# Kernel optimization log

Measured on AMD Instinct MI355X. Metric: run time of the kernel, lower is better.

## Reference

```python
import math
import jax, jax.numpy as jnp
import numpy as np

B, T, H, D = 8, 4096, 8, 64
D_MODEL = H * D  # 512
K = 8            # multiwavelet order k
C = 64           # channel multiplier c (c*k = d_model)
CK = C * K
MODES = 32       # num_modes (alpha)
L = 2            # decomposition levels


def _skft(z, w_re, w_im):
    # sparseKernelFT1d: (B, N, c, k) -> (B, N, c, k)
    b, n, c, k = z.shape
    zf = jnp.fft.rfft(z.reshape(b, n, c * k).transpose(0, 2, 1), axis=-1)  # (b, ck, n//2+1)
    f = n // 2 + 1
    l = min(MODES, f)
    w = w_re[:, :, :l] + 1j * w_im[:, :, :l]
    out = jnp.einsum('bix,iox->box', zf[:, :, :l], w)
    out_ft = jnp.pad(out, ((0, 0), (0, 0), (0, f - l)))  # zero out high modes
    y = jnp.fft.irfft(out_ft, n=n, axis=-1)
    return y.transpose(0, 2, 1).reshape(b, n, c, k)


def _pad_pow2(z):
    n = z.shape[1]
    nl = 2 ** math.ceil(math.log2(n))
    if n == nl:
        return z
    return jnp.concatenate([z, z[:, : nl - n]], axis=1)


def _forward(x, lin_in_w, lin_in_b, lin_out_w, lin_out_b, t0_w, t0_b,
             wA_re, wA_im, wB_re, wB_im, wC_re, wC_im, ec_s, ec_d, rc_e, rc_o):
    b, t, h, d = x.shape
    z = x.reshape(b, t, h * d) @ lin_in_w + lin_in_b  # (b, t, c*k)
    z = z.reshape(b, t, C, K)
    n0 = z.shape[1]
    z = _pad_pow2(z)
    Ud, Us = [], []
    cur = z
    for _ in range(L):  # decompose
        xa = jnp.concatenate([cur[:, ::2], cur[:, 1::2]], axis=-1)  # (b, n/2, c, 2k)
        dcoef = xa @ ec_d  # (b, n/2, c, k)
        scoef = xa @ ec_s
        Ud.append(_skft(dcoef, wA_re, wA_im) + _skft(scoef, wB_re, wB_im))
        Us.append(_skft(dcoef, wC_re, wC_im))
        cur = scoef
    cur = cur @ t0_w + t0_b  # T_0: Linear(k, k) on last dim
    for i in range(L - 1, -1, -1):  # reconstruct, coarsest -> finest
        cur = cur + Us[i]
        cur = jnp.concatenate([cur, Ud[i]], axis=-1)  # (b, n, c, 2k)
        x_e = cur @ rc_e
        x_o = cur @ rc_o
        bb, nn, cc, kk = x_e.shape
        cur = jnp.stack([x_e, x_o], axis=2).reshape(bb, 2 * nn, cc, kk)  # interleave even/odd
    cur = cur[:, :n0]
    out = cur.reshape(b, t, CK) @ lin_out_w + lin_out_b
    return out.reshape(b, t, h, d)


def setup_inputs():
    key = jax.random.key(0)
    ks = jax.random.split(key, 18)
    scale = 1.0 / (CK * CK)  # matches 1/(c*k*c*k)
    u = lambda kk: scale * jax.random.uniform(kk, (CK, CK, MODES), jnp.float32)
    return {
        'x': jax.random.normal(ks[0], (B, T, H, D), jnp.float32),
        'lin_in_w': jax.random.normal(ks[1], (D_MODEL, CK), jnp.float32) * 0.02,
        'lin_in_b': jnp.zeros((CK,), jnp.float32),
        'lin_out_w': jax.random.normal(ks[2], (CK, D_MODEL), jnp.float32) * 0.02,
        'lin_out_b': jnp.zeros((D_MODEL,), jnp.float32),
        't0_w': jax.random.normal(ks[3], (K, K), jnp.float32) * 0.3,
        't0_b': jnp.zeros((K,), jnp.float32),
        'wA_re': u(ks[4]), 'wA_im': u(ks[5]),
        'wB_re': u(ks[6]), 'wB_im': u(ks[7]),
        'wC_re': u(ks[8]), 'wC_im': u(ks[9]),
        'ec_s': jax.random.normal(ks[10], (2 * K, K), jnp.float32) * 0.35,
        'ec_d': jax.random.normal(ks[11], (2 * K, K), jnp.float32) * 0.35,
        'rc_e': jax.random.normal(ks[12], (2 * K, K), jnp.float32) * 0.35,
        'rc_o': jax.random.normal(ks[13], (2 * K, K), jnp.float32) * 0.35,
    }


def reference(x, lin_in_w, lin_in_b, lin_out_w, lin_out_b, t0_w, t0_b,
              wA_re, wA_im, wB_re, wB_im, wC_re, wC_im, ec_s, ec_d, rc_e, rc_o):
    return _forward(x, lin_in_w, lin_in_b, lin_out_w, lin_out_b, t0_w, t0_b,
                    wA_re, wA_im, wB_re, wB_im, wC_re, wC_im, ec_s, ec_d, rc_e, rc_o)
```

## Files before the change

kernel.cpp:

```cpp
#include <hip/hip_runtime.h>
#include <math.h>

constexpr int NB = 8;
constexpr int CKN = 512;
constexpr int NMODE = 32;

typedef __attribute__((ext_vector_type(8))) short short8x;
typedef __attribute__((ext_vector_type(4))) float f32x4;

__device__ inline unsigned short f2bf(float f) {
  union { float f; unsigned u; } v; v.f = f;
  unsigned u = v.u;
  unsigned r = (u + 0x7fffu + ((u >> 16) & 1u)) >> 16;
  return (unsigned short)r;
}

__global__ void build_tables(float* __restrict__ tab, int n) {
  int idx = blockIdx.x * 256 + threadIdx.x;
  if (idx >= n * NMODE) return;
  int t = idx >> 5;
  int x = idx & 31;
  long long tx = ((long long)t * (long long)x) % n;
  double th = 6.28318530717958647692529 * (double)tx / (double)n;
  tab[2 * idx]     = (float)cos(th);
  tab[2 * idx + 1] = (float)sin(th);
}

__global__ __launch_bounds__(256) void gemm_mfma(
    const float* __restrict__ A, const float* __restrict__ W,
    const float* __restrict__ bias, float* __restrict__ C) {
  __shared__ __align__(16) unsigned short As[128 * 40];
  __shared__ __align__(16) unsigned short Bs[128 * 40];
  const int bm = blockIdx.x * 128, bn = blockIdx.y * 128;
  const int tid = threadIdx.x;
  const int wave = tid >> 6, lane = tid & 63;
  const int wm = (wave >> 1) * 64, wn = (wave & 1) * 64;
  const int lm = lane & 15, quad = lane >> 4;

  f32x4 zero = {0.f, 0.f, 0.f, 0.f};
  f32x4 acc[4][4];
#pragma unroll
  for (int i = 0; i < 4; ++i)
#pragma unroll
    for (int j = 0; j < 4; ++j) acc[i][j] = zero;

  for (int k0 = 0; k0 < 512; k0 += 32) {
    __syncthreads();
#pragma unroll
    for (int r = 0; r < 4; ++r) {
      int slot = tid + r * 256;
      int m = slot >> 3, k4 = (slot & 7) << 2;
      float4 v = *(const float4*)&A[(size_t)(bm + m) * 512 + k0 + k4];
      ushort4 u;
      u.x = f2bf(v.x); u.y = f2bf(v.y); u.z = f2bf(v.z); u.w = f2bf(v.w);
      *(ushort4*)&As[m * 40 + k4] = u;
    }
#pragma unroll
    for (int r = 0; r < 4; ++r) {
      int slot = tid + r * 256;
      int n = slot & 127, kg = slot >> 7;
      float w0 = W[(size_t)(k0 + kg * 4 + 0) * 512 + bn + n];
      float w1 = W[(size_t)(k0 + kg * 4 + 1) * 512 + bn + n];
      float w2 = W[(size_t)(k0 + kg * 4 + 2) * 512 + bn + n];
      float w3 = W[(size_t)(k0 + kg * 4 + 3) * 512 + bn + n];
      ushort4 u;
      u.x = f2bf(w0); u.y = f2bf(w1); u.z = f2bf(w2); u.w = f2bf(w3);
      *(ushort4*)&Bs[n * 40 + kg * 4] = u;
    }
    __syncthreads();
    short8x af[4], bf[4];
#pragma unroll
    for (int ti = 0; ti < 4; ++ti)
      af[ti] = *(short8x*)&As[(wm + ti * 16 + lm) * 40 + quad * 8];
#pragma unroll
    for (int tj = 0; tj < 4; ++tj)
      bf[tj] = *(short8x*)&Bs[(wn + tj * 16 + lm) * 40 + quad * 8];
#pragma unroll
    for (int ti = 0; ti < 4; ++ti)
#pragma unroll
      for (int tj = 0; tj < 4; ++tj)
        acc[ti][tj] = __builtin_amdgcn_mfma_f32_16x16x32_bf16(af[ti], bf[tj], acc[ti][tj], 0, 0, 0);
  }
  float bv[4];
#pragma unroll
  for (int tj = 0; tj < 4; ++tj) bv[tj] = bias[bn + wn + tj * 16 + lm];
#pragma unroll
  for (int ti = 0; ti < 4; ++ti)
#pragma unroll
    for (int tj = 0; tj < 4; ++tj)
#pragma unroll
      for (int r = 0; r < 4; ++r)
        C[(size_t)(bm + wm + ti * 16 + quad * 4 + r) * 512 + bn + wn + tj * 16 + lm] =
            acc[ti][tj][r] + bv[tj];
}

__global__ __launch_bounds__(256) void coef_kernel(
    const float* __restrict__ cur, const float* __restrict__ ecd,
    const float* __restrict__ ecs, float* __restrict__ dcoef,
    float* __restrict__ scoef, int nhalf) {
  __shared__ float wd[128], ws2[128];
  int tid = threadIdx.x;
  if (tid < 128) { wd[tid] = ecd[tid]; ws2[tid] = ecs[tid]; }
  __syncthreads();
  size_t idx = (size_t)blockIdx.x * 256 + tid;
  int c = (int)(idx & 63);
  int t = (int)((idx >> 6) % (size_t)nhalf);
  int b = (int)(idx / ((size_t)nhalf * 64));
  const float* r0 = cur + ((size_t)b * nhalf * 2 + 2 * (size_t)t) * CKN + c * 8;
  float xa[16];
  *(float4*)&xa[0]  = *(const float4*)&r0[0];
  *(float4*)&xa[4]  = *(const float4*)&r0[4];
  *(float4*)&xa[8]  = *(const float4*)&r0[CKN];
  *(float4*)&xa[12] = *(const float4*)&r0[CKN + 4];
  float d[8] = {}, s[8] = {};
#pragma unroll
  for (int j = 0; j < 16; ++j) {
    float v = xa[j];
#pragma unroll
    for (int k = 0; k < 8; ++k) {
      d[k] += v * wd[j * 8 + k];
      s[k] += v * ws2[j * 8 + k];
    }
  }
  size_t o = ((size_t)b * nhalf + t) * CKN + c * 8;
  *(float4*)&dcoef[o]     = *(float4*)&d[0];
  *(float4*)&dcoef[o + 4] = *(float4*)&d[4];
  *(float4*)&scoef[o]     = *(float4*)&s[0];
  *(float4*)&scoef[o + 4] = *(float4*)&s[4];
}

__global__ __launch_bounds__(256) void fwd_dft_partial(
    const float* __restrict__ in, const float* __restrict__ tab,
    float* __restrict__ part, int n) {
  __shared__ float ltab[64 * 64];
  const int p = blockIdx.x, b = blockIdx.y;
  const int P = gridDim.x;
  const int tid = threadIdx.x;
  for (int i = tid; i < 4096; i += 256) ltab[i] = tab[(size_t)p * 4096 + i];
  __syncthreads();
  float ar0[NMODE] = {}, ai0[NMODE] = {}, ar1[NMODE] = {}, ai1[NMODE] = {};
  const float* src = in + ((size_t)b * n + (size_t)p * 64) * CKN + 2 * tid;
#pragma unroll 2
  for (int t = 0; t < 64; ++t) {
    float2 v = *(const float2*)&src[(size_t)t * CKN];
    const float* tr = &ltab[t * 64];
#pragma unroll
    for (int x = 0; x < NMODE; ++x) {
      float c = tr[2 * x], sn = tr[2 * x + 1];
      ar0[x] += v.x * c; ai0[x] -= v.x * sn;
      ar1[x] += v.y * c; ai1[x] -= v.y * sn;
    }
  }
  float* pr = part + ((size_t)b * P + p) * NMODE * CKN + 2 * tid;
  float* pi = pr + (size_t)NB * P * NMODE * CKN;
#pragma unroll
  for (int x = 0; x < NMODE; ++x) {
    float2 r; r.x = ar0[x]; r.y = ar1[x];
    float2 im; im.x = ai0[x]; im.y = ai1[x];
    *(float2*)&pr[(size_t)x * CKN] = r;
    *(float2*)&pi[(size_t)x * CKN] = im;
  }
}

__global__ __launch_bounds__(256) void dft_reduce(
    const float* __restrict__ part, float* __restrict__ fre,
    float* __restrict__ fim, int P) {
  int idx = blockIdx.x * 256 + threadIdx.x;
  int ck = idx & 511;
  int x = (idx >> 9) & 31;
  int b = idx >> 14;
  size_t base = ((size_t)b * P * NMODE + x) * CKN + ck;
  size_t ip = (size_t)NB * P * NMODE * CKN;
  size_t ps = (size_t)NMODE * CKN;
  float sr = 0.f, si = 0.f;
  for (int p = 0; p < P; ++p) { sr += part[base + p * ps]; si += part[base + ip + p * ps]; }
  fre[idx] = sr;
  fim[idx] = si;
}

__global__ __launch_bounds__(256) void mode_mul(
    const float* __restrict__ freq,
    const float* __restrict__ wAre, const float* __restrict__ wAim,
    const float* __restrict__ wBre, const float* __restrict__ wBim,
    const float* __restrict__ wCre, const float* __restrict__ wCim,
    float* __restrict__ mpart) {
  __shared__ __align__(16) float lf[4096];
  const int otile = blockIdx.x, chunk = blockIdx.y;
  const int tid = threadIdx.x;
  const int x = tid & 31, ol = tid >> 5;
  const int o = otile * 8 + ol;
  const int i0 = chunk * 32;
  float acc[2][8][4] = {};
  for (int ii = 0; ii < 32; ii += 4) {
    float wv[4][6];
    size_t wo0 = ((size_t)(i0 + ii) * 512 + o) * 32 + x;
#pragma unroll
    for (int i = 0; i < 4; ++i) {
      size_t wo = wo0 + (size_t)i * 16384;
      wv[i][0] = wAre[wo]; wv[i][1] = wAim[wo];
      wv[i][2] = wBre[wo]; wv[i][3] = wBim[wo];
      wv[i][4] = wCre[wo]; wv[i][5] = wCim[wo];
    }
    __syncthreads();
#pragma unroll
    for (int j = 0; j < 16; ++j) {
      int idx = tid + j * 256;
      int il = idx & 3, xx = (idx >> 2) & 31, bb = (idx >> 7) & 7;
      int pl = (idx >> 10) & 3, lv = idx >> 12;
      lf[(((lv * 8 + bb) * 4 + il) * 32 + xx) * 4 + pl] =
          freq[(size_t)(lv * 4 + pl) * 131072 + ((size_t)bb * 32 + xx) * 512 + i0 + ii + il];
    }
    __syncthreads();
#pragma unroll
    for (int i = 0; i < 4; ++i) {
      float aR = wv[i][0], aI = wv[i][1];
      float bR = wv[i][2], bI = wv[i][3];
      float cR = wv[i][4], cI = wv[i][5];
#pragma unroll
      for (int lv = 0; lv < 2; ++lv)
#pragma unroll
        for (int bq = 0; bq < 8; ++bq) {
          float4 f = *(float4*)&lf[(((lv * 8 + bq) * 4 + i) * 32 + x) * 4];
          acc[lv][bq][0] += f.x * aR - f.y * aI + f.z * bR - f.w * bI;
          acc[lv][bq][1] += f.x * aI + f.y * aR + f.z * bI + f.w * bR;
          acc[lv][bq][2] += f.x * cR - f.y * cI;
          acc[lv][bq][3] += f.x * cI + f.y * cR;
        }
    }
  }
#pragma unroll
  for (int lv = 0; lv < 2; ++lv)
#pragma unroll
    for (int bq = 0; bq < 8; ++bq) {
      float4 v;
      v.x = acc[lv][bq][0]; v.y = acc[lv][bq][1];
      v.z = acc[lv][bq][2]; v.w = acc[lv][bq][3];
      *(float4*)&mpart[((((size_t)lv * 16 + chunk) * 8 + bq) * 32 + x) * 2048 + o * 4] = v;
    }
}

__global__ __launch_bounds__(256) void mm_reduce(
    const float* __restrict__ mpart, float* __restrict__ outplanes) {
  int idx = blockIdx.x * 256 + threadIdx.x;
  int o = idx & 511;
  int x = (idx >> 9) & 31;
  int b = (idx >> 14) & 7;
  int lvl = idx >> 17;
  float s0 = 0, s1 = 0, s2 = 0, s3 = 0;
  for (int ch = 0; ch < 16; ++ch) {
    const float4 v = *(const float4*)&mpart[((((size_t)lvl * 16 + ch) * 8 + b) * 32 + x) * 2048 + o * 4];
    s0 += v.x; s1 += v.y; s2 += v.z; s3 += v.w;
  }
  size_t fo = ((size_t)b * 32 + x) * 512 + o;
  float* bp = outplanes + (size_t)lvl * 4 * 131072;
  bp[fo] = s0;
  bp[131072 + fo] = s1;
  bp[262144 + fo] = s2;
  bp[393216 + fo] = s3;
}

__global__ __launch_bounds__(256) void t0_kernel(
    float* __restrict__ cur, const float* __restrict__ w,
    const float* __restrict__ bvec, int rows) {
  __shared__ float lw[64];
  __shared__ float lb[8];
  int tid = threadIdx.x;
  if (tid < 64) lw[tid] = w[tid];
  if (tid < 8) lb[tid] = bvec[tid];
  __syncthreads();
  size_t r = (size_t)blockIdx.x * 256 + tid;
  if (r >= (size_t)rows) return;
  float* p = cur + r * 8;
  float in[8];
  *(float4*)&in[0] = *(const float4*)&p[0];
  *(float4*)&in[4] = *(const float4*)&p[4];
  float outv[8];
#pragma unroll
  for (int k2 = 0; k2 < 8; ++k2) {
    float a = lb[k2];
#pragma unroll
    for (int k = 0; k < 8; ++k) a += in[k] * lw[k * 8 + k2];
    outv[k2] = a;
  }
  *(float4*)&p[0] = *(float4*)&outv[0];
  *(float4*)&p[4] = *(float4*)&outv[4];
}

__global__ __launch_bounds__(256) void inv_dft(
    const float* __restrict__ fre, const float* __restrict__ fim,
    const float* __restrict__ tab, float* __restrict__ out,
    int n, int beta) {
  __shared__ float ltab[512];
  const int tg = blockIdx.x, b = blockIdx.y;
  const int tid = threadIdx.x;
  for (int i = tid; i < 512; i += 256) ltab[i] = tab[(size_t)tg * 512 + i];
  __syncthreads();
  const int o = tid * 2;
  const float invn = 1.0f / (float)n;
  float fr0[NMODE], fi0[NMODE], fr1[NMODE], fi1[NMODE];
  const float* pr = fre + (size_t)b * NMODE * CKN + o;
  const float* pi = fim + (size_t)b * NMODE * CKN + o;
#pragma unroll
  for (int x = 0; x < NMODE; ++x) {
    float w = (x == 0) ? invn : 2.0f * invn;
    float2 r = *(const float2*)&pr[(size_t)x * CKN];
    float2 im = *(const float2*)&pi[(size_t)x * CKN];
    fr0[x] = r.x * w; fr1[x] = r.y * w;
    fi0[x] = im.x * w; fi1[x] = im.y * w;
  }
  float* dst = out + ((size_t)b * n + (size_t)tg * 8) * CKN + o;
#pragma unroll
  for (int t = 0; t < 8; ++t) {
    const float* tr = &ltab[t * 64];
    float y0 = 0.f, y1 = 0.f;
#pragma unroll
    for (int x = 0; x < NMODE; ++x) {
      float c = tr[2 * x], sn = tr[2 * x + 1];
      y0 += fr0[x] * c - fi0[x] * sn;
      y1 += fr1[x] * c - fi1[x] * sn;
    }
    float2* dp = (float2*)&dst[(size_t)t * CKN];
    float2 yy;
    if (beta) { float2 prev = *dp; yy.x = prev.x + y0; yy.y = prev.y + y1; }
    else { yy.x = y0; yy.y = y1; }
    *dp = yy;
  }
}

__global__ __launch_bounds__(256) void recon_kernel(
    const float* __restrict__ cur, const float* __restrict__ ud,
    const float* __restrict__ rce, const float* __restrict__ rco,
    float* __restrict__ out, int n) {
  __shared__ float we[128], wo[128];
  int tid = threadIdx.x;
  if (tid < 128) { we[tid] = rce[tid]; wo[tid] = rco[tid]; }
  __syncthreads();
  size_t idx = (size_t)blockIdx.x * 256 + tid;
  int c = (int)(idx & 63);
  int t = (int)((idx >> 6) % (size_t)n);
  int b = (int)(idx / ((size_t)n * 64));
  size_t off = ((size_t)b * n + t) * CKN + c * 8;
  float cat[16];
  *(float4*)&cat[0]  = *(const float4*)&cur[off];
  *(float4*)&cat[4]  = *(const float4*)&cur[off + 4];
  *(float4*)&cat[8]  = *(const float4*)&ud[off];
  *(float4*)&cat[12] = *(const float4*)&ud[off + 4];
  float xe[8] = {}, xo[8] = {};
#pragma unroll
  for (int j = 0; j < 16; ++j) {
    float v = cat[j];
#pragma unroll
    for (int k = 0; k < 8; ++k) {
      xe[k] += v * we[j * 8 + k];
      xo[k] += v * wo[j * 8 + k];
    }
  }
  size_t po = ((size_t)b * 2 * n + 2 * (size_t)t) * CKN + c * 8;
  *(float4*)&out[po]           = *(float4*)&xe[0];
  *(float4*)&out[po + 4]       = *(float4*)&xe[4];
  *(float4*)&out[po + CKN]     = *(float4*)&xo[0];
  *(float4*)&out[po + CKN + 4] = *(float4*)&xo[4];
}

extern "C" void kernel_launch(void* const* d_in, const int* in_sizes, int n_in,
                              void* d_out, int out_size, void* d_ws, size_t ws_size,
                              hipStream_t stream) {
  (void)in_sizes; (void)n_in; (void)out_size; (void)ws_size;
  const float* x         = (const float*)d_in[0];
  const float* lin_in_w  = (const float*)d_in[1];
  const float* lin_in_b  = (const float*)d_in[2];
  const float* lin_out_w = (const float*)d_in[3];
  const float* lin_out_b = (const float*)d_in[4];
  const float* t0_w      = (const float*)d_in[5];
  const float* t0_b      = (const float*)d_in[6];
  const float* wAre      = (const float*)d_in[7];
  const float* wAim      = (const float*)d_in[8];
  const float* wBre      = (const float*)d_in[9];
  const float* wBim      = (const float*)d_in[10];
  const float* wCre      = (const float*)d_in[11];
  const float* wCim      = (const float*)d_in[12];
  const float* ec_s      = (const float*)d_in[13];
  const float* ec_d      = (const float*)d_in[14];
  const float* rc_e      = (const float*)d_in[15];
  const float* rc_o      = (const float*)d_in[16];
  float* ws = (float*)d_ws;
  float* out = (float*)d_out;

  float* Z    = ws + 0;
  float* D0   = ws + 16777216;
  float* S0   = ws + 25165824;
  float* D1   = ws + 33554432;
  float* S1   = ws + 37748736;
  float* F0   = ws + 41943040;
  float* TAB2 = ws + 44040192;
  float* TAB1 = ws + 44171264;
  float* PART = Z;
  float* MMP  = Z;

  build_tables<<<(2048 * NMODE + 255) / 256, 256, 0, stream>>>(TAB2, 2048);
  build_tables<<<(1024 * NMODE + 255) / 256, 256, 0, stream>>>(TAB1, 1024);

  gemm_mfma<<<dim3(256, 4), 256, 0, stream>>>(x, lin_in_w, lin_in_b, Z);

  coef_kernel<<<(NB * 2048 * 64) / 256, 256, 0, stream>>>(Z, ec_d, ec_s, D0, S0, 2048);

  fwd_dft_partial<<<dim3(32, NB), 256, 0, stream>>>(D0, TAB2, PART, 2048);
  dft_reduce<<<512, 256, 0, stream>>>(PART, F0 + 0 * 131072, F0 + 1 * 131072, 32);
  fwd_dft_partial<<<dim3(32, NB), 256, 0, stream>>>(S0, TAB2, PART, 2048);
  dft_reduce<<<512, 256, 0, stream>>>(PART, F0 + 2 * 131072, F0 + 3 * 131072, 32);

  coef_kernel<<<(NB * 1024 * 64) / 256, 256, 0, stream>>>(S0, ec_d, ec_s, D1, S1, 1024);

  fwd_dft_partial<<<dim3(16, NB), 256, 0, stream>>>(D1, TAB1, PART, 1024);
  dft_reduce<<<512, 256, 0, stream>>>(PART, F0 + 4 * 131072, F0 + 5 * 131072, 16);
  fwd_dft_partial<<<dim3(16, NB), 256, 0, stream>>>(S1, TAB1, PART, 1024);
  dft_reduce<<<512, 256, 0, stream>>>(PART, F0 + 6 * 131072, F0 + 7 * 131072, 16);

  mode_mul<<<dim3(64, 16), 256, 0, stream>>>(F0, wAre, wAim, wBre, wBim, wCre, wCim, MMP);
  mm_reduce<<<1024, 256, 0, stream>>>(MMP, F0 + 8 * 131072);

  t0_kernel<<<(NB * 1024 * 64) / 256, 256, 0, stream>>>(S1, t0_w, t0_b, NB * 1024 * 64);

  inv_dft<<<dim3(128, NB), 256, 0, stream>>>(F0 + 14 * 131072, F0 + 15 * 131072, TAB1, S1, 1024, 1);
  inv_dft<<<dim3(128, NB), 256, 0, stream>>>(F0 + 12 * 131072, F0 + 13 * 131072, TAB1, D1, 1024, 0);
  recon_kernel<<<(NB * 1024 * 64) / 256, 256, 0, stream>>>(S1, D1, rc_e, rc_o, S0, 1024);

  inv_dft<<<dim3(256, NB), 256, 0, stream>>>(F0 + 10 * 131072, F0 + 11 * 131072, TAB2, S0, 2048, 1);
  inv_dft<<<dim3(256, NB), 256, 0, stream>>>(F0 + 8 * 131072, F0 + 9 * 131072, TAB2, D0, 2048, 0);
  recon_kernel<<<(NB * 2048 * 64) / 256, 256, 0, stream>>>(S0, D0, rc_e, rc_o, Z, 2048);

  gemm_mfma<<<dim3(256, 4), 256, 0, stream>>>(Z, lin_out_w, lin_out_b, out);
}
```

Measured before the change: 899.1 us.

## Replace twiddle tables with on-the-fly rotation recurrences and retile DFT and mode-mul kernels

```diff
diff --git a/kernel.cpp b/kernel.cpp
--- a/kernel.cpp
+++ b/kernel.cpp
@@ -4,6 +4,7 @@
 constexpr int NB = 8;
 constexpr int CKN = 512;
 constexpr int NMODE = 32;
+constexpr int NCH = 8;
 
 typedef __attribute__((ext_vector_type(8))) short short8x;
 typedef __attribute__((ext_vector_type(4))) float f32x4;
@@ -13,17 +14,6 @@
   unsigned u = v.u;
   unsigned r = (u + 0x7fffu + ((u >> 16) & 1u)) >> 16;
   return (unsigned short)r;
-}
-
-__global__ void build_tables(float* __restrict__ tab, int n) {
-  int idx = blockIdx.x * 256 + threadIdx.x;
-  if (idx >= n * NMODE) return;
-  int t = idx >> 5;
-  int x = idx & 31;
-  long long tx = ((long long)t * (long long)x) % n;
-  double th = 6.28318530717958647692529 * (double)tx / (double)n;
-  tab[2 * idx]     = (float)cos(th);
-  tab[2 * idx + 1] = (float)sin(th);
 }
 
 __global__ __launch_bounds__(256) void gemm_mfma(
@@ -129,37 +119,42 @@
   *(float4*)&scoef[o + 4] = *(float4*)&s[4];
 }
 
-__global__ __launch_bounds__(256) void fwd_dft_partial(
-    const float* __restrict__ in, const float* __restrict__ tab,
-    float* __restrict__ part, int n) {
-  __shared__ float ltab[64 * 64];
-  const int p = blockIdx.x, b = blockIdx.y;
+__global__ __launch_bounds__(256) void fwd_dft(
+    const float* __restrict__ in, float* __restrict__ part, int n) {
+  const int p = blockIdx.x, b = blockIdx.y, cb = blockIdx.z;
   const int P = gridDim.x;
   const int tid = threadIdx.x;
-  for (int i = tid; i < 4096; i += 256) ltab[i] = tab[(size_t)p * 4096 + i];
-  __syncthreads();
-  float ar0[NMODE] = {}, ai0[NMODE] = {}, ar1[NMODE] = {}, ai1[NMODE] = {};
-  const float* src = in + ((size_t)b * n + (size_t)p * 64) * CKN + 2 * tid;
-#pragma unroll 2
+  const int cs = tid & 7, x = tid >> 3;
+  const int ck = cb * 64 + cs * 8;
+  const int t0 = p * 64;
+  float c, s, cstep, sstep;
+  float a0 = -6.28318530717958647692f * (float)((x * t0) % n) / (float)n;
+  __sincosf(a0, &s, &c);
+  float a1 = -6.28318530717958647692f * (float)x / (float)n;
+  __sincosf(a1, &sstep, &cstep);
+  float ar[8] = {}, ai[8] = {};
+  const float* src = in + ((size_t)b * n + t0) * CKN + ck;
   for (int t = 0; t < 64; ++t) {
-    float2 v = *(const float2*)&src[(size_t)t * CKN];
-    const float* tr = &ltab[t * 64];
-#pragma unroll
-    for (int x = 0; x < NMODE; ++x) {
-      float c = tr[2 * x], sn = tr[2 * x + 1];
-      ar0[x] += v.x * c; ai0[x] -= v.x * sn;
-      ar1[x] += v.y * c; ai1[x] -= v.y * sn;
-    }
-  }
-  float* pr = part + ((size_t)b * P + p) * NMODE * CKN + 2 * tid;
+    float4 v0 = *(const float4*)&src[(size_t)t * CKN];
+    float4 v1 = *(const float4*)&src[(size_t)t * CKN + 4];
+    ar[0] += v0.x * c; ai[0] += v0.x * s;
+    ar[1] += v0.y * c; ai[1] += v0.y * s;
+    ar[2] += v0.z * c; ai[2] += v0.z * s;
+    ar[3] += v0.w * c; ai[3] += v0.w * s;
+    ar[4] += v1.x * c; ai[4] += v1.x * s;
+    ar[5] += v1.y * c; ai[5] += v1.y * s;
+    ar[6] += v1.z * c; ai[6] += v1.z * s;
+    ar[7] += v1.w * c; ai[7] += v1.w * s;
+    float cn = c * cstep - s * sstep;
+    float sn = c * sstep + s * cstep;
+    c = cn; s = sn;
+  }
+  float* pr = part + (((size_t)b * P + p) * NMODE + x) * CKN + ck;
   float* pi = pr + (size_t)NB * P * NMODE * CKN;
-#pragma unroll
-  for (int x = 0; x < NMODE; ++x) {
-    float2 r; r.x = ar0[x]; r.y = ar1[x];
-    float2 im; im.x = ai0[x]; im.y = ai1[x];
-    *(float2*)&pr[(size_t)x * CKN] = r;
-    *(float2*)&pi[(size_t)x * CKN] = im;
-  }
+  *(float4*)&pr[0] = *(float4*)&ar[0];
+  *(float4*)&pr[4] = *(float4*)&ar[4];
+  *(float4*)&pi[0] = *(float4*)&ai[0];
+  *(float4*)&pi[4] = *(float4*)&ai[4];
 }
 
 __global__ __launch_bounds__(256) void dft_reduce(
@@ -184,71 +179,84 @@
     const float* __restrict__ wBre, const float* __restrict__ wBim,
     const float* __restrict__ wCre, const float* __restrict__ wCim,
     float* __restrict__ mpart) {
-  __shared__ __align__(16) float lf[4096];
+  __shared__ __align__(16) float lf[8192];
   const int otile = blockIdx.x, chunk = blockIdx.y;
   const int tid = threadIdx.x;
-  const int x = tid & 31, ol = tid >> 5;
-  const int o = otile * 8 + ol;
-  const int i0 = chunk * 32;
-  float acc[2][8][4] = {};
-  for (int ii = 0; ii < 32; ii += 4) {
-    float wv[4][6];
-    size_t wo0 = ((size_t)(i0 + ii) * 512 + o) * 32 + x;
-#pragma unroll
-    for (int i = 0; i < 4; ++i) {
-      size_t wo = wo0 + (size_t)i * 16384;
-      wv[i][0] = wAre[wo]; wv[i][1] = wAim[wo];
-      wv[i][2] = wBre[wo]; wv[i][3] = wBim[wo];
-      wv[i][4] = wCre[wo]; wv[i][5] = wCim[wo];
-    }
+  const int wave = tid >> 6, lane = tid & 63;
+  const int x = lane & 31, og = lane >> 5;
+  const int r0 = wave * 4;
+  const int i0 = chunk * 64;
+  const int o0 = otile * 4 + og * 2;
+  const int sx = tid & 31, spl = (tid >> 5) & 3, srp = tid >> 7;
+  float acc[4][2][4] = {};
+  for (int ii = 0; ii < 64; ii += 4) {
     __syncthreads();
 #pragma unroll
-    for (int j = 0; j < 16; ++j) {
-      int idx = tid + j * 256;
-      int il = idx & 3, xx = (idx >> 2) & 31, bb = (idx >> 7) & 7;
-      int pl = (idx >> 10) & 3, lv = idx >> 12;
-      lf[(((lv * 8 + bb) * 4 + il) * 32 + xx) * 4 + pl] =
-          freq[(size_t)(lv * 4 + pl) * 131072 + ((size_t)bb * 32 + xx) * 512 + i0 + ii + il];
+    for (int j = 0; j < 8; ++j) {
+      int row = srp * 8 + j;
+      int lv = row >> 3, bb = row & 7;
+      float4 v = *(const float4*)&freq[(size_t)(lv * 4 + spl) * 131072 +
+                                       ((size_t)bb * 32 + sx) * 512 + i0 + ii];
+      *(float4*)&lf[((row * 4 + spl) * 32 + sx) * 4] = v;
     }
     __syncthreads();
-#pragma unroll
-    for (int i = 0; i < 4; ++i) {
-      float aR = wv[i][0], aI = wv[i][1];
-      float bR = wv[i][2], bI = wv[i][3];
-      float cR = wv[i][4], cI = wv[i][5];
-#pragma unroll
-      for (int lv = 0; lv < 2; ++lv)
-#pragma unroll
-        for (int bq = 0; bq < 8; ++bq) {
-          float4 f = *(float4*)&lf[(((lv * 8 + bq) * 4 + i) * 32 + x) * 4];
-          acc[lv][bq][0] += f.x * aR - f.y * aI + f.z * bR - f.w * bI;
-          acc[lv][bq][1] += f.x * aI + f.y * aR + f.z * bI + f.w * bR;
-          acc[lv][bq][2] += f.x * cR - f.y * cI;
-          acc[lv][bq][3] += f.x * cI + f.y * cR;
+    float wv[4][2][6];
+#pragma unroll
+    for (int i = 0; i < 4; ++i)
+#pragma unroll
+      for (int o = 0; o < 2; ++o) {
+        size_t wo = ((size_t)(i0 + ii + i) * 512 + (o0 + o)) * 32 + x;
+        wv[i][o][0] = wAre[wo]; wv[i][o][1] = wAim[wo];
+        wv[i][o][2] = wBre[wo]; wv[i][o][3] = wBim[wo];
+        wv[i][o][4] = wCre[wo]; wv[i][o][5] = wCim[wo];
+      }
+#pragma unroll
+    for (int r = 0; r < 4; ++r) {
+      int row = r0 + r;
+      float4 qdR = *(float4*)&lf[((row * 4 + 0) * 32 + x) * 4];
+      float4 qdI = *(float4*)&lf[((row * 4 + 1) * 32 + x) * 4];
+      float4 qsR = *(float4*)&lf[((row * 4 + 2) * 32 + x) * 4];
+      float4 qsI = *(float4*)&lf[((row * 4 + 3) * 32 + x) * 4];
+      const float* adR = (const float*)&qdR;
+      const float* adI = (const float*)&qdI;
+      const float* asR = (const float*)&qsR;
+      const float* asI = (const float*)&qsI;
+#pragma unroll
+      for (int i = 0; i < 4; ++i) {
+        float dR = adR[i], dI = adI[i], sR = asR[i], sI = asI[i];
+#pragma unroll
+        for (int o = 0; o < 2; ++o) {
+          acc[r][o][0] += dR * wv[i][o][0] - dI * wv[i][o][1] + sR * wv[i][o][2] - sI * wv[i][o][3];
+          acc[r][o][1] += dR * wv[i][o][1] + dI * wv[i][o][0] + sR * wv[i][o][3] + sI * wv[i][o][2];
+          acc[r][o][2] += dR * wv[i][o][4] - dI * wv[i][o][5];
+          acc[r][o][3] += dR * wv[i][o][5] + dI * wv[i][o][4];
         }
-    }
-  }
-#pragma unroll
-  for (int lv = 0; lv < 2; ++lv)
-#pragma unroll
-    for (int bq = 0; bq < 8; ++bq) {
+      }
+    }
+  }
+#pragma unroll
+  for (int r = 0; r < 4; ++r) {
+    int row = r0 + r;
+    int lv = row >> 3, bb = row & 7;
+#pragma unroll
+    for (int o = 0; o < 2; ++o) {
       float4 v;
-      v.x = acc[lv][bq][0]; v.y = acc[lv][bq][1];
-      v.z = acc[lv][bq][2]; v.w = acc[lv][bq][3];
-      *(float4*)&mpart[((((size_t)lv * 16 + chunk) * 8 + bq) * 32 + x) * 2048 + o * 4] = v;
-    }
+      v.x = acc[r][o][0]; v.y = acc[r][o][1]; v.z = acc[r][o][2]; v.w = acc[r][o][3];
+      *(float4*)&mpart[((((size_t)lv * NCH + chunk) * 8 + bb) * 512 + (o0 + o)) * 128 + (size_t)x * 4] = v;
+    }
+  }
 }
 
 __global__ __launch_bounds__(256) void mm_reduce(
     const float* __restrict__ mpart, float* __restrict__ outplanes) {
   int idx = blockIdx.x * 256 + threadIdx.x;
-  int o = idx & 511;
-  int x = (idx >> 9) & 31;
+  int x = idx & 31;
+  int o = (idx >> 5) & 511;
   int b = (idx >> 14) & 7;
   int lvl = idx >> 17;
   float s0 = 0, s1 = 0, s2 = 0, s3 = 0;
-  for (int ch = 0; ch < 16; ++ch) {
-    const float4 v = *(const float4*)&mpart[((((size_t)lvl * 16 + ch) * 8 + b) * 32 + x) * 2048 + o * 4];
+  for (int ch = 0; ch < NCH; ++ch) {
+    const float4 v = *(const float4*)&mpart[((((size_t)lvl * NCH + ch) * 8 + b) * 512 + o) * 128 + (size_t)x * 4];
     s0 += v.x; s1 += v.y; s2 += v.z; s3 += v.w;
   }
   size_t fo = ((size_t)b * 32 + x) * 512 + o;
@@ -288,42 +296,46 @@
 
 __global__ __launch_bounds__(256) void inv_dft(
     const float* __restrict__ fre, const float* __restrict__ fim,
-    const float* __restrict__ tab, float* __restrict__ out,
-    int n, int beta) {
-  __shared__ float ltab[512];
-  const int tg = blockIdx.x, b = blockIdx.y;
-  const int tid = threadIdx.x;
-  for (int i = tid; i < 512; i += 256) ltab[i] = tab[(size_t)tg * 512 + i];
-  __syncthreads();
-  const int o = tid * 2;
+    float* __restrict__ out, int n, int beta) {
+  const int tb = blockIdx.x, b = blockIdx.y, chh = blockIdx.z;
+  const int ck = chh * 256 + threadIdx.x;
   const float invn = 1.0f / (float)n;
-  float fr0[NMODE], fi0[NMODE], fr1[NMODE], fi1[NMODE];
-  const float* pr = fre + (size_t)b * NMODE * CKN + o;
-  const float* pi = fim + (size_t)b * NMODE * CKN + o;
-#pragma unroll
-  for (int x = 0; x < NMODE; ++x) {
-    float w = (x == 0) ? invn : 2.0f * invn;
-    float2 r = *(const float2*)&pr[(size_t)x * CKN];
-    float2 im = *(const float2*)&pi[(size_t)x * CKN];
-    fr0[x] = r.x * w; fr1[x] = r.y * w;
-    fi0[x] = im.x * w; fi1[x] = im.y * w;
-  }
-  float* dst = out + ((size_t)b * n + (size_t)tg * 8) * CKN + o;
-#pragma unroll
-  for (int t = 0; t < 8; ++t) {
-    const float* tr = &ltab[t * 64];
-    float y0 = 0.f, y1 = 0.f;
-#pragma unroll
-    for (int x = 0; x < NMODE; ++x) {
-      float c = tr[2 * x], sn = tr[2 * x + 1];
-      y0 += fr0[x] * c - fi0[x] * sn;
-      y1 += fr1[x] * c - fi1[x] * sn;
-    }
-    float2* dp = (float2*)&dst[(size_t)t * CKN];
-    float2 yy;
-    if (beta) { float2 prev = *dp; yy.x = prev.x + y0; yy.y = prev.y + y1; }
-    else { yy.x = y0; yy.y = y1; }
-    *dp = yy;
+  float fr[NMODE], fi[NMODE];
+  const float* pr = fre + (size_t)b * NMODE * CKN + ck;
+  const float* pi = fim + (size_t)b * NMODE * CKN + ck;
+#pragma unroll
+  for (int xx = 0; xx < NMODE; ++xx) {
+    float w = (xx == 0) ? invn : 2.0f * invn;
+    fr[xx] = pr[(size_t)xx * CKN] * w;
+    fi[xx] = pi[(size_t)xx * CKN] * w;
+  }
+  float* dst = out + ((size_t)b * n + (size_t)tb * 64) * CKN + ck;
+  for (int tt = 0; tt < 32; ++tt) {
+    int ta = tb * 64 + tt;
+    int tb2 = ta + 32;
+    float cA, sA, c1A, s1A, cB, sB, c1B, s1B;
+    __sincosf(6.28318530717958647692f * (float)ta / (float)n, &s1A, &c1A);
+    __sincosf(6.28318530717958647692f * (float)tb2 / (float)n, &s1B, &c1B);
+    cA = 1.f; sA = 0.f; cB = 1.f; sB = 0.f;
+    float yA = 0.f, yB = 0.f;
+#pragma unroll
+    for (int xx = 0; xx < NMODE; ++xx) {
+      yA += fr[xx] * cA - fi[xx] * sA;
+      yB += fr[xx] * cB - fi[xx] * sB;
+      float cnA = cA * c1A - sA * s1A;
+      float snA = cA * s1A + sA * c1A;
+      cA = cnA; sA = snA;
+      float cnB = cB * c1B - sB * s1B;
+      float snB = cB * s1B + sB * c1B;
+      cB = cnB; sB = snB;
+    }
+    if (beta) {
+      dst[(size_t)tt * CKN] += yA;
+      dst[(size_t)(tt + 32) * CKN] += yB;
+    } else {
+      dst[(size_t)tt * CKN] = yA;
+      dst[(size_t)(tt + 32) * CKN] = yB;
+    }
   }
 }
 
@@ -392,41 +404,36 @@
   float* D1   = ws + 33554432;
   float* S1   = ws + 37748736;
   float* F0   = ws + 41943040;
-  float* TAB2 = ws + 44040192;
-  float* TAB1 = ws + 44171264;
   float* PART = Z;
   float* MMP  = Z;
 
-  build_tables<<<(2048 * NMODE + 255) / 256, 256, 0, stream>>>(TAB2, 2048);
-  build_tables<<<(1024 * NMODE + 255) / 256, 256, 0, stream>>>(TAB1, 1024);
-
   gemm_mfma<<<dim3(256, 4), 256, 0, stream>>>(x, lin_in_w, lin_in_b, Z);
 
   coef_kernel<<<(NB * 2048 * 64) / 256, 256, 0, stream>>>(Z, ec_d, ec_s, D0, S0, 2048);
 
-  fwd_dft_partial<<<dim3(32, NB), 256, 0, stream>>>(D0, TAB2, PART, 2048);
+  fwd_dft<<<dim3(32, NB, 8), 256, 0, stream>>>(D0, PART, 2048);
   dft_reduce<<<512, 256, 0, stream>>>(PART, F0 + 0 * 131072, F0 + 1 * 131072, 32);
-  fwd_dft_partial<<<dim3(32, NB), 256, 0, stream>>>(S0, TAB2, PART, 2048);
+  fwd_dft<<<dim3(32, NB, 8), 256, 0, stream>>>(S0, PART, 2048);
   dft_reduce<<<512, 256, 0, stream>>>(PART, F0 + 2 * 131072, F0 + 3 * 131072, 32);
 
   coef_kernel<<<(NB * 1024 * 64) / 256, 256, 0, stream>>>(S0, ec_d, ec_s, D1, S1, 1024);
 
-  fwd_dft_partial<<<dim3(16, NB), 256, 0, stream>>>(D1, TAB1, PART, 1024);
+  fwd_dft<<<dim3(16, NB, 8), 256, 0, stream>>>(D1, PART, 1024);
   dft_reduce<<<512, 256, 0, stream>>>(PART, F0 + 4 * 131072, F0 + 5 * 131072, 16);
-  fwd_dft_partial<<<dim3(16, NB), 256, 0, stream>>>(S1, TAB1, PART, 1024);
+  fwd_dft<<<dim3(16, NB, 8), 256, 0, stream>>>(S1, PART, 1024);
   dft_reduce<<<512, 256, 0, stream>>>(PART, F0 + 6 * 131072, F0 + 7 * 131072, 16);
 
-  mode_mul<<<dim3(64, 16), 256, 0, stream>>>(F0, wAre, wAim, wBre, wBim, wCre, wCim, MMP);
+  mode_mul<<<dim3(128, NCH), 256, 0, stream>>>(F0, wAre, wAim, wBre, wBim, wCre, wCim, MMP);
   mm_reduce<<<1024, 256, 0, stream>>>(MMP, F0 + 8 * 131072);
 
   t0_kernel<<<(NB * 1024 * 64) / 256, 256, 0, stream>>>(S1, t0_w, t0_b, NB * 1024 * 64);
 
-  inv_dft<<<dim3(128, NB), 256, 0, stream>>>(F0 + 14 * 131072, F0 + 15 * 131072, TAB1, S1, 1024, 1);
-  inv_dft<<<dim3(128, NB), 256, 0, stream>>>(F0 + 12 * 131072, F0 + 13 * 131072, TAB1, D1, 1024, 0);
+  inv_dft<<<dim3(16, NB, 2), 256, 0, stream>>>(F0 + 14 * 131072, F0 + 15 * 131072, S1, 1024, 1);
+  inv_dft<<<dim3(16, NB, 2), 256, 0, stream>>>(F0 + 12 * 131072, F0 + 13 * 131072, D1, 1024, 0);
   recon_kernel<<<(NB * 1024 * 64) / 256, 256, 0, stream>>>(S1, D1, rc_e, rc_o, S0, 1024);
 
-  inv_dft<<<dim3(256, NB), 256, 0, stream>>>(F0 + 10 * 131072, F0 + 11 * 131072, TAB2, S0, 2048, 1);
-  inv_dft<<<dim3(256, NB), 256, 0, stream>>>(F0 + 8 * 131072, F0 + 9 * 131072, TAB2, D0, 2048, 0);
+  inv_dft<<<dim3(32, NB, 2), 256, 0, stream>>>(F0 + 10 * 131072, F0 + 11 * 131072, S0, 2048, 1);
+  inv_dft<<<dim3(32, NB, 2), 256, 0, stream>>>(F0 + 8 * 131072, F0 + 9 * 131072, D0, 2048, 0);
   recon_kernel<<<(NB * 2048 * 64) / 256, 256, 0, stream>>>(S0, D0, rc_e, rc_o, Z, 2048);
 
   gemm_mfma<<<dim3(256, 4), 256, 0, stream>>>(Z, lin_out_w, lin_out_b, out);
```

Measured after the change: 931.2 us. 3.6% more time.
